# Kernel optimization log

Hardware: AMD Instinct MI355X
Metric: run time of the kernel (lower is better)

Reference implementation:

```python
import jax, jax.numpy as jnp
import numpy as np

MAX_THRESHOLD = 0.95


def leaky_clamp(x, lo, hi, slope):
    # identity inside [lo, hi], linear with `slope` outside
    return jnp.where(x < lo, lo + slope * (x - lo),
                     jnp.where(x > hi, hi + slope * (x - hi), x))


def or_gate_layer(x, W, tau_adder):
    # x: (B, in), W: (out, in)
    in_f = W.shape[1]
    tau_floor = float(np.log(in_f - 1) + np.log(MAX_THRESHOLD) - np.log(1.0 - MAX_THRESHOLD))
    tau = tau_floor + jax.nn.leaky_relu(tau_adder, negative_slope=0.05)
    aw = leaky_clamp(W, 0.0, 1.0, 0.1)           # (out, in)
    z = x[:, None, :] * aw[None, :, :]           # (B, out, in) broadcast
    p = jax.nn.softmax(tau * z, axis=-1)         # tau-scaled softmax over in
    return jnp.sum(p * z, axis=-1)               # (B, out)


def setup_inputs() -> dict:
    key = jax.random.key(0)
    ks = jax.random.split(key, 9)
    input_dim = 512
    layer_dims = [1024, 512, 256, 128]
    x = jax.random.uniform(ks[0], (128, input_dim), dtype=jnp.float32)
    in_dim = input_dim * 2
    out = {"x": x}
    for i, out_dim in enumerate(layer_dims):
        out[f"W{i}"] = jax.random.normal(ks[1 + i], (out_dim, in_dim), dtype=jnp.float32)
        out[f"tau{i}"] = jnp.zeros((), dtype=jnp.float32)
        in_dim = out_dim  # only_inverter=True
    return out


def reference(x, W0, W1, W2, W3, tau0, tau1, tau2, tau3):
    h = jnp.concatenate([x, 1.0 - x], axis=-1)   # pass_invert
    for W, t in ((W0, tau0), (W1, tau1), (W2, tau2), (W3, tau3)):
        h = 1.0 - or_gate_layer(h, W, t)         # only_inverter: invert after every layer
    return h
```

## Files before the change

### kernel.cpp

```cpp
#include <hip/hip_runtime.h>
#include <math.h>

#if defined(__has_builtin)
#  if __has_builtin(__builtin_amdgcn_exp2f)
#    define EXP2F(x) __builtin_amdgcn_exp2f(x)
#  endif
#endif
#ifndef EXP2F
#  define EXP2F(x) __expf(0.69314718055994530942f * (x))
#endif

__device__ __forceinline__ float fast_exp2(float x) {
  const float M = 12582912.0f;
  const float y = x + M;
  const float n = y - M;
  const float f = x - n;
  float p = fmaf(f, 0.055504109f, 0.24022651f);
  p = fmaf(f, p, 0.69314718f);
  p = fmaf(f, p, 1.0f);
  const int r = (__float_as_int(y) << 23) + __float_as_int(p);
  return __int_as_float(r);
}

template <int IN, int OUT, int BB, bool FIRST>
__launch_bounds__(256)
__global__ void or_layer(const float* __restrict__ hin,
                         const float* __restrict__ W,
                         const float* __restrict__ tau_ptr,
                         float* __restrict__ hout,
                         float tau_floor) {
  constexpr int OBB = 2;
  constexpr int NIT = IN / 64;
  constexpr int nOT = OUT / 32;

  const int lane = threadIdx.x & 63;
  const int wid  = threadIdx.x >> 6;
  const int il   = lane & 15;
  const int og   = lane >> 4;

  const int ot = blockIdx.x % nOT;
  const int bt = blockIdx.x / nOT;
  const int b0 = bt * BB;
  const int o0 = ot * 32 + wid * 8 + og * OBB;

  const float ta  = tau_ptr[0];
  const float tau = tau_floor + (ta >= 0.0f ? ta : 0.05f * ta);
  const float c2  = tau * 1.44269504088896340736f;

  const float4* __restrict__ Wv = (const float4*)W;
  const float4* __restrict__ Hv = (const float4*)hin;

  float s[BB][OBB], t[BB][OBB];
#pragma unroll
  for (int r = 0; r < BB; ++r)
#pragma unroll
    for (int c = 0; c < OBB; ++c) { s[r][c] = 0.0f; t[r][c] = 0.0f; }

#pragma unroll 2
  for (int ic = 0; ic < NIT; ++ic) {
    const int i4 = ic * 16 + il;

    float hc[BB][4];
    if (FIRST) {
      constexpr int HALF4 = IN / 8;
      if (i4 < HALF4) {
#pragma unroll
        for (int r = 0; r < BB; ++r) {
          float4 v = Hv[(b0 + r) * HALF4 + i4];
          hc[r][0] = v.x; hc[r][1] = v.y; hc[r][2] = v.z; hc[r][3] = v.w;
        }
      } else {
#pragma unroll
        for (int r = 0; r < BB; ++r) {
          float4 v = Hv[(b0 + r) * HALF4 + (i4 - HALF4)];
          hc[r][0] = 1.0f - v.x; hc[r][1] = 1.0f - v.y;
          hc[r][2] = 1.0f - v.z; hc[r][3] = 1.0f - v.w;
        }
      }
    } else {
#pragma unroll
      for (int r = 0; r < BB; ++r) {
        float4 v = Hv[(b0 + r) * (IN / 4) + i4];
        hc[r][0] = v.x; hc[r][1] = v.y; hc[r][2] = v.z; hc[r][3] = v.w;
      }
    }

    float cw[OBB][4];
#pragma unroll
    for (int c = 0; c < OBB; ++c) {
      float4 v = Wv[(o0 + c) * (IN / 4) + i4];
      float wj[4] = {v.x, v.y, v.z, v.w};
#pragma unroll
      for (int j = 0; j < 4; ++j) {
        const float m  = fminf(fmaxf(wj[j], 0.0f), 1.0f);
        const float aw = fmaf(0.1f, wj[j] - m, m);
        cw[c][j] = c2 * aw;
      }
    }

#pragma unroll
    for (int r = 0; r < BB; ++r)
#pragma unroll
      for (int c = 0; c < OBB; ++c)
#pragma unroll
        for (int j = 0; j < 4; ++j) {
          const float arg = cw[c][j] * hc[r][j];
          const float e = (j & 1) ? fast_exp2(arg) : EXP2F(arg);
          s[r][c] += e;
          t[r][c]  = fmaf(arg, e, t[r][c]);
        }
  }

#pragma unroll
  for (int m = 1; m < 16; m <<= 1) {
#pragma unroll
    for (int r = 0; r < BB; ++r)
#pragma unroll
      for (int c = 0; c < OBB; ++c) {
        s[r][c] += __shfl_xor(s[r][c], m, 64);
        t[r][c] += __shfl_xor(t[r][c], m, 64);
      }
  }

  if (il == 0) {
    const float inv_c2 = 1.0f / c2;
#pragma unroll
    for (int r = 0; r < BB; ++r)
#pragma unroll
      for (int c = 0; c < OBB; ++c) {
        const float out = t[r][c] / s[r][c] * inv_c2;
        hout[(b0 + r) * OUT + (o0 + c)] = 1.0f - out;
      }
  }
}

extern "C" void kernel_launch(void* const* d_in, const int* in_sizes, int n_in,
                              void* d_out, int out_size, void* d_ws, size_t ws_size,
                              hipStream_t stream) {
  const float* x    = (const float*)d_in[0];
  const float* W0   = (const float*)d_in[1];
  const float* tau0 = (const float*)d_in[2];
  const float* W1   = (const float*)d_in[3];
  const float* tau1 = (const float*)d_in[4];
  const float* W2   = (const float*)d_in[5];
  const float* tau2 = (const float*)d_in[6];
  const float* W3   = (const float*)d_in[7];
  const float* tau3 = (const float*)d_in[8];

  float* h1  = (float*)d_ws;
  float* h2  = h1 + 128 * 1024;
  float* h3  = h2 + 128 * 512;
  float* out = (float*)d_out;

  const double LOGR = 2.9444389791664403;
  const float tf1024 = (float)(log(1023.0) + LOGR);
  const float tf512  = (float)(log(511.0)  + LOGR);
  const float tf256  = (float)(log(255.0)  + LOGR);

  or_layer<1024, 1024, 4, true ><<<1024, 256, 0, stream>>>(x,  W0, tau0, h1,  tf1024);
  or_layer<1024,  512, 4, false><<< 512, 256, 0, stream>>>(h1, W1, tau1, h2,  tf1024);
  or_layer< 512,  256, 2, false><<< 512, 256, 0, stream>>>(h2, W2, tau2, h3,  tf512);
  or_layer< 256,  128, 1, false><<< 512, 256, 0, stream>>>(h3, W3, tau3, out, tf256);
}
```

Measured before the change: 125.3 us.

## Stage activations in LDS, prefetch weights, retune batch tiles and occupancy

Each block now loads its batch rows of activations into shared memory once, building the inverted half there for the first layer. Weight float4 loads are software-prefetched one iteration ahead. Layers 2 and 3 use smaller batch tiles with twice the blocks, and launch bounds request 4 blocks per CU. The aim is to cut redundant global activation loads and hide weight-load latency, at the cost of a block barrier, extra LDS use, and more register pressure from the prefetch.

```diff
diff --git a/kernel.cpp b/kernel.cpp
--- a/kernel.cpp
+++ b/kernel.cpp
@@ -23,7 +23,7 @@
 }
 
 template <int IN, int OUT, int BB, bool FIRST>
-__launch_bounds__(256)
+__launch_bounds__(256, 4)
 __global__ void or_layer(const float* __restrict__ hin,
                          const float* __restrict__ W,
                          const float* __restrict__ tau_ptr,
@@ -32,9 +32,13 @@
   constexpr int OBB = 2;
   constexpr int NIT = IN / 64;
   constexpr int nOT = OUT / 32;
+  constexpr int IN4 = IN / 4;
 
-  const int lane = threadIdx.x & 63;
-  const int wid  = threadIdx.x >> 6;
+  __shared__ float4 lds_h[BB][IN4];
+
+  const int tid  = threadIdx.x;
+  const int lane = tid & 63;
+  const int wid  = tid >> 6;
   const int il   = lane & 15;
   const int og   = lane >> 4;
 
@@ -50,51 +54,60 @@
   const float4* __restrict__ Wv = (const float4*)W;
   const float4* __restrict__ Hv = (const float4*)hin;
 
+  if (FIRST) {
+    constexpr int HALF4 = IN / 8;
+    for (int idx = tid; idx < BB * HALF4; idx += 256) {
+      const int r = idx / HALF4;
+      const int k = idx - r * HALF4;
+      const float4 v = Hv[(b0 + r) * HALF4 + k];
+      lds_h[r][k] = v;
+      lds_h[r][HALF4 + k] =
+          make_float4(1.0f - v.x, 1.0f - v.y, 1.0f - v.z, 1.0f - v.w);
+    }
+  } else {
+    for (int idx = tid; idx < BB * IN4; idx += 256) {
+      const int r = idx / IN4;
+      const int k = idx - r * IN4;
+      lds_h[r][k] = Hv[(b0 + r) * IN4 + k];
+    }
+  }
+  __syncthreads();
+
   float s[BB][OBB], t[BB][OBB];
 #pragma unroll
   for (int r = 0; r < BB; ++r)
 #pragma unroll
     for (int c = 0; c < OBB; ++c) { s[r][c] = 0.0f; t[r][c] = 0.0f; }
 
+  const float4* wp0 = Wv + (size_t)(o0 + 0) * IN4 + il;
+  const float4* wp1 = Wv + (size_t)(o0 + 1) * IN4 + il;
+
+  float4 wcur0 = wp0[0];
+  float4 wcur1 = wp1[0];
+
 #pragma unroll 2
   for (int ic = 0; ic < NIT; ++ic) {
-    const int i4 = ic * 16 + il;
+    const int icn = (ic + 1 < NIT) ? (ic + 1) : (NIT - 1);
+    const float4 wnxt0 = wp0[icn * 16];
+    const float4 wnxt1 = wp1[icn * 16];
 
     float hc[BB][4];
-    if (FIRST) {
-      constexpr int HALF4 = IN / 8;
-      if (i4 < HALF4) {
 #pragma unroll
-        for (int r = 0; r < BB; ++r) {
-          float4 v = Hv[(b0 + r) * HALF4 + i4];
-          hc[r][0] = v.x; hc[r][1] = v.y; hc[r][2] = v.z; hc[r][3] = v.w;
-        }
-      } else {
-#pragma unroll
-        for (int r = 0; r < BB; ++r) {
-          float4 v = Hv[(b0 + r) * HALF4 + (i4 - HALF4)];
-          hc[r][0] = 1.0f - v.x; hc[r][1] = 1.0f - v.y;
-          hc[r][2] = 1.0f - v.z; hc[r][3] = 1.0f - v.w;
-        }
-      }
-    } else {
-#pragma unroll
-      for (int r = 0; r < BB; ++r) {
-        float4 v = Hv[(b0 + r) * (IN / 4) + i4];
-        hc[r][0] = v.x; hc[r][1] = v.y; hc[r][2] = v.z; hc[r][3] = v.w;
-      }
+    for (int r = 0; r < BB; ++r) {
+      const float4 v = lds_h[r][ic * 16 + il];
+      hc[r][0] = v.x; hc[r][1] = v.y; hc[r][2] = v.z; hc[r][3] = v.w;
     }
 
     float cw[OBB][4];
-#pragma unroll
-    for (int c = 0; c < OBB; ++c) {
-      float4 v = Wv[(o0 + c) * (IN / 4) + i4];
-      float wj[4] = {v.x, v.y, v.z, v.w};
+    {
+      const float wj0[4] = {wcur0.x, wcur0.y, wcur0.z, wcur0.w};
+      const float wj1[4] = {wcur1.x, wcur1.y, wcur1.z, wcur1.w};
 #pragma unroll
       for (int j = 0; j < 4; ++j) {
-        const float m  = fminf(fmaxf(wj[j], 0.0f), 1.0f);
-        const float aw = fmaf(0.1f, wj[j] - m, m);
-        cw[c][j] = c2 * aw;
+        float m  = fminf(fmaxf(wj0[j], 0.0f), 1.0f);
+        cw[0][j] = c2 * fmaf(0.1f, wj0[j] - m, m);
+        m        = fminf(fmaxf(wj1[j], 0.0f), 1.0f);
+        cw[1][j] = c2 * fmaf(0.1f, wj1[j] - m, m);
       }
     }
 
@@ -109,10 +122,13 @@
           s[r][c] += e;
           t[r][c]  = fmaf(arg, e, t[r][c]);
         }
+
+    wcur0 = wnxt0;
+    wcur1 = wnxt1;
   }
 
 #pragma unroll
-  for (int m = 1; m < 16; m <<= 1) {
+  for (int m = 1; m < 16; m <<= 1)
 #pragma unroll
     for (int r = 0; r < BB; ++r)
 #pragma unroll
@@ -120,7 +136,6 @@
         s[r][c] += __shfl_xor(s[r][c], m, 64);
         t[r][c] += __shfl_xor(t[r][c], m, 64);
       }
-  }
 
   if (il == 0) {
     const float inv_c2 = 1.0f / c2;
@@ -158,7 +173,7 @@
   const float tf256  = (float)(log(255.0)  + LOGR);
 
   or_layer<1024, 1024, 4, true ><<<1024, 256, 0, stream>>>(x,  W0, tau0, h1,  tf1024);
-  or_layer<1024,  512, 4, false><<< 512, 256, 0, stream>>>(h1, W1, tau1, h2,  tf1024);
-  or_layer< 512,  256, 2, false><<< 512, 256, 0, stream>>>(h2, W2, tau2, h3,  tf512);
+  or_layer<1024,  512, 2, false><<<1024, 256, 0, stream>>>(h1, W1, tau1, h2,  tf1024);
+  or_layer< 512,  256, 1, false><<<1024, 256, 0, stream>>>(h2, W2, tau2, h3,  tf512);
   or_layer< 256,  128, 1, false><<< 512, 256, 0, stream>>>(h3, W3, tau3, out, tf256);
 }
```

Measured after the change: 123.8 us. About the same (-1.2%).
